# Optimization experiments

Measured on AMD Instinct MI355X. Metric: run time of the kernel, lower is better.

Reference implementation:

```python
import jax, jax.numpy as jnp
import numpy as np

B, N, N_IN, MSG_HID, MSG_OUT, N_HID, N_OUT, K = 32, 128, 16, 64, 64, 64, 16, 4
E = N * (N - 1)  # 16256 directed edges, fully connected w/o self-loops


def setup_inputs() -> dict:
    key = jax.random.key(0)
    ks = jax.random.split(key, 8)
    # one-hot relation matrices (NRI convention)
    rows, cols = np.where(np.ones((N, N)) - np.eye(N))
    eye = np.eye(N, dtype=np.float32)
    rel_rec = jnp.asarray(eye[rows])   # [E, N]
    rel_send = jnp.asarray(eye[cols])  # [E, N]
    s = 0.1  # weight init scale
    return {
        "inputs": jax.random.normal(ks[0], (B, N_IN, N), jnp.float32),
        "rel_rec": rel_rec,
        "rel_send": rel_send,
        "rel_types": jax.nn.softmax(jax.random.normal(ks[1], (B, E, K), jnp.float32), axis=-1),
        "W1": jax.random.normal(ks[2], (K, 2 * N_IN, MSG_HID), jnp.float32) * s,
        "b1": jnp.zeros((K, MSG_HID), jnp.float32),
        "W2": jax.random.normal(ks[3], (K, MSG_HID, MSG_OUT), jnp.float32) * s,
        "b2": jnp.zeros((K, MSG_OUT), jnp.float32),
        "Wo1": jax.random.normal(ks[4], (MSG_OUT + N_IN, N_HID), jnp.float32) * s,
        "bo1": jnp.zeros((N_HID,), jnp.float32),
        "Wo2": jax.random.normal(ks[5], (N_HID, N_HID), jnp.float32) * s,
        "bo2": jnp.zeros((N_HID,), jnp.float32),
        "Wo3": jax.random.normal(ks[6], (N_HID, N_OUT), jnp.float32) * s,
        "bo3": jnp.zeros((N_OUT,), jnp.float32),
    }


def reference(inputs, rel_rec, rel_send, rel_types, W1, b1, W2, b2, Wo1, bo1, Wo2, bo2, Wo3, bo3):
    x = jnp.transpose(inputs, (0, 2, 1))                     # [B, N, n_in]
    senders = jnp.einsum('en,bnf->bef', rel_send, x)          # [B, E, n_in]
    receivers = jnp.einsum('en,bnf->bef', rel_rec, x)         # [B, E, n_in]
    pre_msg = jnp.concatenate([senders, receivers], axis=-1)  # [B, E, 2*n_in]
    all_msgs = jnp.zeros((pre_msg.shape[0], pre_msg.shape[1], W2.shape[-1]), pre_msg.dtype)
    for k in range(W1.shape[0]):  # small fixed loop over edge types
        m = jax.nn.relu(pre_msg @ W1[k] + b1[k])
        m = jax.nn.relu(m @ W2[k] + b2[k])
        all_msgs = all_msgs + m * rel_types[:, :, k:k + 1]
    # edge2node aggregation (no normalization in forward path, matches source)
    agg_msgs = jnp.einsum('bem,en->bnm', all_msgs, rel_rec)   # [B, N, msg_out]
    aug_msgs = jnp.concatenate([x, agg_msgs], axis=-1)        # [B, N, n_in+msg_out]
    h = jax.nn.relu(aug_msgs @ Wo1 + bo1)  # dropout disabled (eval mode)
    h = jax.nn.relu(h @ Wo2 + bo2)
    pred = h @ Wo3 + bo3                                      # [B, N, n_out]
    return jnp.transpose(pred, (0, 2, 1))                     # [B, n_out, N]
```

## Files before the change

kernel.cpp:

```cpp
#include <hip/hip_runtime.h>
#include <stdint.h>

#define B_  32
#define N_  128
#define NIN 16
#define K_  4
#define E_  (N_*(N_-1))

typedef float    f4 __attribute__((ext_vector_type(4)));
typedef _Float16 h8 __attribute__((ext_vector_type(8)));
typedef _Float16 h4 __attribute__((ext_vector_type(4)));

__global__ __launch_bounds__(256) void prep(
    const float* __restrict__ inp, const float* __restrict__ W1,
    const float* __restrict__ b1,  const float* __restrict__ W2,
    const float* __restrict__ Wo1, const float* __restrict__ Wo2,
    const float* __restrict__ Wo3, const float* __restrict__ rt,
    _Float16* __restrict__ Sh, _Float16* __restrict__ Rh,
    _Float16* __restrict__ w2h, _Float16* __restrict__ wn,
    float* __restrict__ rtf)
{
    const int bid = blockIdx.x;
    const int tid = threadIdx.x;
    if (bid < 1024) {
        int gid = bid*256 + tid;
        int c0 = (gid & 15)*4;
        int n  = (gid >> 4) & 127;
        int b  = (gid >> 11) & 31;
        int k  = gid >> 16;
        f4 s = {0.f,0.f,0.f,0.f};
        f4 r = *(const f4*)(b1 + k*64 + c0);
        const float* xp  = inp + (b*NIN)*N_ + n;
        const f4* w1s = (const f4*)(W1 + (k*32)*64 + c0);
        const f4* w1r = (const f4*)(W1 + (k*32 + 16)*64 + c0);
        #pragma unroll
        for (int f = 0; f < 16; ++f) {
            float xv = xp[f*N_];
            s += xv * w1s[f*16];
            r += xv * w1r[f*16];
        }
        int base = ((k*B_ + b)*N_ + n)*64 + c0;
        h4 sh, rh;
        #pragma unroll
        for (int u = 0; u < 4; ++u) { sh[u] = (_Float16)s[u]; rh[u] = (_Float16)r[u]; }
        *(h4*)(Sh + base) = sh;
        *(h4*)(Rh + base) = rh;
    } else if (bid < 1088) {
        int t = (bid - 1024)*256 + tid;
        int i    = t & 7;
        int lane = (t >> 3) & 63;
        int nt   = (t >> 9) & 3;
        int ks   = (t >> 11) & 1;
        int k    = t >> 12;
        int c = ks*32 + (lane >> 4)*8 + i;
        int o = nt*16 + (lane & 15);
        w2h[t] = (_Float16)W2[(k*64 + c)*64 + o];
    } else if (bid < 1132) {
        int t = (bid - 1088)*256 + tid;
        int j    = t & 7;
        int lane = (t >> 3) & 63;
        int f    = t >> 9;
        int col = lane & 15, q = lane >> 4, row = q*8 + j;
        float v;
        if (f < 12) {
            int ks = f >> 2, nt = f & 3, i = ks*32 + row;
            v = (i < 80) ? Wo1[i*64 + nt*16 + col] : 0.f;
        } else if (f < 20) {
            int g = f - 12, ks = g >> 2, nt = g & 3, i = ks*32 + row;
            v = Wo2[i*64 + nt*16 + col];
        } else {
            int ks = f - 20, i = ks*32 + row;
            v = Wo3[i*16 + col];
        }
        wn[t] = (_Float16)v;
    } else {
        int t = (bid - 1132)*256 + tid;
        int jg = t & 31;
        int r  = (t >> 5) & 127;
        int b  = t >> 12;
        const f4* rt4p = (const f4*)(rt + (size_t)(b*E_ + r*127)*4);
        #pragma unroll
        for (int u = 0; u < 4; ++u) {
            int j = jg*4 + u;
            if (j < 127) {
                f4 v = rt4p[j];
                int s = j + (j >= r ? 1 : 0);
                #pragma unroll
                for (int k = 0; k < 4; ++k)
                    rtf[(size_t)((k*B_ + b)*N_ + r)*N_ + s] = v[k];
            } else {
                #pragma unroll
                for (int k = 0; k < 4; ++k)
                    rtf[(size_t)((k*B_ + b)*N_ + r)*N_ + r] = 0.f;
            }
        }
    }
}

__global__ __launch_bounds__(256) void edge_mfma(
    const _Float16* __restrict__ Sh, const _Float16* __restrict__ Rh,
    const _Float16* __restrict__ w2h, const float* __restrict__ rtf,
    const float* __restrict__ b2, float* __restrict__ aggK)
{
    __shared__ _Float16 Rlh[16*64];
    __shared__ float    Rtf[16*128];
    __shared__ float    aggW[2][2][8][64];

    const int tid  = threadIdx.x;
    const int wave = tid >> 6;
    const int lane = tid & 63;
    const int col  = lane & 15;
    const int q    = lane >> 4;
    const int h    = wave & 1;
    const int p    = wave >> 1;
    const int bid  = blockIdx.x;
    const int re   = bid & 7;
    const int b    = (bid >> 3) & 31;
    const int k    = bid >> 8;
    const int kb   = k*B_ + b;
    const int r0   = re*16;

    if (tid < 128)
        *(h8*)(Rlh + tid*8) = *(const h8*)(Rh + ((size_t)kb*N_ + r0)*64 + tid*8);
    {
        const float* src = rtf + ((size_t)kb*N_ + r0)*N_;
        *(f4*)(Rtf + tid*4)        = *(const f4*)(src + tid*4);
        *(f4*)(Rtf + 1024 + tid*4) = *(const f4*)(src + 1024 + tid*4);
    }

    h8 sf[4][2];
    const _Float16* Sg = Sh + ((size_t)kb*N_ + h*64)*64;
    #pragma unroll
    for (int mt = 0; mt < 4; ++mt) {
        sf[mt][0] = *(const h8*)(Sg + (mt*16 + col)*64 + q*8);
        sf[mt][1] = *(const h8*)(Sg + (mt*16 + col)*64 + (4 + q)*8);
    }

    const h8* w2v = (const h8*)w2h;
    h8 w2f[2][4];
    #pragma unroll
    for (int ks = 0; ks < 2; ++ks)
        #pragma unroll
        for (int nt = 0; nt < 4; ++nt)
            w2f[ks][nt] = w2v[((k*2 + ks)*4 + nt)*64 + lane];

    f4 b2i[4];
    #pragma unroll
    for (int nt = 0; nt < 4; ++nt) {
        float v = b2[k*64 + nt*16 + col];
        b2i[nt][0] = v; b2i[nt][1] = v; b2i[nt][2] = v; b2i[nt][3] = v;
    }

    __syncthreads();

    const h8 zero8 = {0,0,0,0,0,0,0,0};
    const f4 zero4 = {0.f,0.f,0.f,0.f};

    #pragma unroll 1
    for (int rg = 0; rg < 8; ++rg) {
        const int rl = p*8 + rg;
        h8 rf0 = *(const h8*)(Rlh + rl*64 + q*8);
        h8 rf1 = *(const h8*)(Rlh + rl*64 + (4 + q)*8);

        f4 vacc[4] = {zero4, zero4, zero4, zero4};
        #pragma unroll
        for (int mt = 0; mt < 4; ++mt) {
            f4 rt4 = *(const f4*)(Rtf + rl*128 + h*64 + mt*16 + q*4);
            h8 a0 = __builtin_elementwise_max(sf[mt][0] + rf0, zero8);
            h8 a1 = __builtin_elementwise_max(sf[mt][1] + rf1, zero8);

            #pragma unroll
            for (int nt = 0; nt < 4; ++nt) {
                f4 acc = __builtin_amdgcn_mfma_f32_16x16x32_f16(a0, w2f[0][nt], b2i[nt], 0, 0, 0);
                acc     = __builtin_amdgcn_mfma_f32_16x16x32_f16(a1, w2f[1][nt], acc,    0, 0, 0);
                f4 m = __builtin_elementwise_max(acc, zero4);
                vacc[nt] += rt4 * m;
            }
        }
        #pragma unroll
        for (int nt = 0; nt < 4; ++nt) {
            float v = vacc[nt][0] + vacc[nt][1] + vacc[nt][2] + vacc[nt][3];
            v += __shfl_xor(v, 16, 64);
            v += __shfl_xor(v, 32, 64);
            if (lane < 16) aggW[p][h][rg][nt*16 + lane] = v;
        }
    }
    __syncthreads();

    {
        int rl = tid >> 4, c4 = tid & 15;
        f4 v = *(const f4*)(&aggW[rl >> 3][0][rl & 7][c4*4])
             + *(const f4*)(&aggW[rl >> 3][1][rl & 7][c4*4]);
        *(f4*)(aggK + ((size_t)kb*N_ + r0 + rl)*64 + c4*4) = v;
    }
}

__global__ __launch_bounds__(256) void node_mfma(
    const float* __restrict__ aggK, const float* __restrict__ inp,
    const _Float16* __restrict__ wn,
    const float* __restrict__ bo1, const float* __restrict__ bo2,
    const float* __restrict__ bo3, float* __restrict__ out)
{
    __shared__ _Float16 augH[64*128];
    __shared__ _Float16 h12[64*64];

    const int tid = threadIdx.x;
    const int b   = blockIdx.x >> 1;
    const int r0  = (blockIdx.x & 1)*64;

    {
        const int nl = tid >> 2, c4 = tid & 3;
        const int r  = r0 + nl;
        float xv[4];
        #pragma unroll
        for (int u = 0; u < 4; ++u)
            xv[u] = inp[(b*NIN + c4*4 + u)*N_ + r];
        f4 av[4];
        #pragma unroll
        for (int w = 0; w < 4; ++w) {
            int c = w*16 + c4*4;
            f4 a = {0.f,0.f,0.f,0.f};
            #pragma unroll
            for (int k = 0; k < 4; ++k)
                a += *(const f4*)(aggK + (((size_t)k*B_ + b)*N_ + r)*64 + c);
            av[w] = a;
        }
        #pragma unroll
        for (int u = 0; u < 4; ++u) {
            int i = c4*4 + u;
            augH[nl*128 + (((i>>3) ^ (nl&15))<<3) + (i&7)] = (_Float16)xv[u];
        }
        #pragma unroll
        for (int w = 0; w < 4; ++w)
            #pragma unroll
            for (int u = 0; u < 4; ++u) {
                int i = 16 + w*16 + c4*4 + u;
                augH[nl*128 + (((i>>3) ^ (nl&15))<<3) + (i&7)] = (_Float16)av[w][u];
            }
        if (c4 < 2)
            #pragma unroll
            for (int u = 0; u < 8; ++u) {
                int i = 80 + c4*8 + u;
                augH[nl*128 + (((i>>3) ^ (nl&15))<<3) + (i&7)] = (_Float16)0.f;
            }
    }
    __syncthreads();

    const int mt  = tid >> 6, lane = tid & 63;
    const int col = lane & 15, q = lane >> 4;
    const h8* wv   = (const h8*)wn;
    const h8* augV = (const h8*)augH;
    const h8* hv   = (const h8*)h12;
    const int nl   = mt*16 + col;

    f4 acc[4];
    #pragma unroll
    for (int nt = 0; nt < 4; ++nt) {
        float v = bo1[nt*16 + col];
        acc[nt][0] = v; acc[nt][1] = v; acc[nt][2] = v; acc[nt][3] = v;
    }
    #pragma unroll
    for (int ks = 0; ks < 3; ++ks) {
        h8 af = augV[nl*16 + ((ks*4 + q) ^ col)];
        #pragma unroll
        for (int nt = 0; nt < 4; ++nt)
            acc[nt] = __builtin_amdgcn_mfma_f32_16x16x32_f16(af, wv[(ks*4 + nt)*64 + lane], acc[nt], 0, 0, 0);
    }
    #pragma unroll
    for (int nt = 0; nt < 4; ++nt)
        #pragma unroll
        for (int i = 0; i < 4; ++i) {
            int n2 = mt*16 + q*4 + i, o = nt*16 + col;
            h12[n2*64 + (((o>>3) ^ (n2&7))<<3) + (o&7)] = (_Float16)fmaxf(acc[nt][i], 0.f);
        }

    f4 acc2[4];
    #pragma unroll
    for (int nt = 0; nt < 4; ++nt) {
        float v = bo2[nt*16 + col];
        acc2[nt][0] = v; acc2[nt][1] = v; acc2[nt][2] = v; acc2[nt][3] = v;
    }
    #pragma unroll
    for (int ks = 0; ks < 2; ++ks) {
        h8 af = hv[nl*8 + ((ks*4 + q) ^ (col & 7))];
        #pragma unroll
        for (int nt = 0; nt < 4; ++nt)
            acc2[nt] = __builtin_amdgcn_mfma_f32_16x16x32_f16(af, wv[(12 + ks*4 + nt)*64 + lane], acc2[nt], 0, 0, 0);
    }
    #pragma unroll
    for (int nt = 0; nt < 4; ++nt)
        #pragma unroll
        for (int i = 0; i < 4; ++i) {
            int n2 = mt*16 + q*4 + i, o = nt*16 + col;
            h12[n2*64 + (((o>>3) ^ (n2&7))<<3) + (o&7)] = (_Float16)fmaxf(acc2[nt][i], 0.f);
        }

    f4 acc3;
    {
        float v = bo3[col];
        acc3[0] = v; acc3[1] = v; acc3[2] = v; acc3[3] = v;
    }
    #pragma unroll
    for (int ks = 0; ks < 2; ++ks) {
        h8 af = hv[nl*8 + ((ks*4 + q) ^ (col & 7))];
        acc3 = __builtin_amdgcn_mfma_f32_16x16x32_f16(af, wv[(20 + ks)*64 + lane], acc3, 0, 0, 0);
    }
    #pragma unroll
    for (int i = 0; i < 4; ++i) {
        int r = r0 + mt*16 + q*4 + i;
        out[(b*NIN + col)*N_ + r] = acc3[i];
    }
}

extern "C" void kernel_launch(void* const* d_in, const int* in_sizes, int n_in,
                              void* d_out, int out_size, void* d_ws, size_t ws_size,
                              hipStream_t stream)
{
    const float* inp = (const float*)d_in[0];
    const float* rt  = (const float*)d_in[3];
    const float* W1  = (const float*)d_in[4];
    const float* b1  = (const float*)d_in[5];
    const float* W2  = (const float*)d_in[6];
    const float* b2  = (const float*)d_in[7];
    const float* Wo1 = (const float*)d_in[8];
    const float* bo1 = (const float*)d_in[9];
    const float* Wo2 = (const float*)d_in[10];
    const float* bo2 = (const float*)d_in[11];
    const float* Wo3 = (const float*)d_in[12];
    const float* bo3 = (const float*)d_in[13];

    _Float16* Sh   = (_Float16*)d_ws;
    _Float16* Rh   = Sh + (1u << 20);
    _Float16* w2h  = Rh + (1u << 20);
    _Float16* wn   = w2h + 16384;
    float*    rtf  = (float*)(wn + 11264);
    float*    aggK = rtf + (1u << 21);

    hipLaunchKernelGGL(prep, dim3(1644), dim3(256), 0, stream,
                       inp, W1, b1, W2, Wo1, Wo2, Wo3, rt, Sh, Rh, w2h, wn, rtf);
    hipLaunchKernelGGL(edge_mfma, dim3(1024), dim3(256), 0, stream,
                       Sh, Rh, w2h, rtf, b2, aggK);
    hipLaunchKernelGGL(node_mfma, dim3(64), dim3(256), 0, stream,
                       aggK, inp, wn, bo1, bo2, bo3, (float*)d_out);
}
```

Measured before the change: 134.6 us.

## Fuse prep stage into edge and node kernels, recompute projections per block

Removes the separate prep kernel and its global-memory intermediates (fp16 sender/receiver projections, repacked weights and the scattered rel_types tensor). Each edge block now stages x, W1 and W2 in shared memory, computes the first-layer projections with MFMA, and scatters rel_types straight into LDS. The node kernel transposes and converts its own weights into LDS. This saves a launch and global round-trips, but every block redundantly recomputes the sender projections and weight conversions, and uses more LDS, which may lower occupancy.

```diff
diff --git a/kernel.cpp b/kernel.cpp
--- a/kernel.cpp
+++ b/kernel.cpp
@@ -9,100 +9,18 @@
 
 typedef float    f4 __attribute__((ext_vector_type(4)));
 typedef _Float16 h8 __attribute__((ext_vector_type(8)));
-typedef _Float16 h4 __attribute__((ext_vector_type(4)));
-
-__global__ __launch_bounds__(256) void prep(
+
+__global__ __launch_bounds__(256) void edge_fused(
     const float* __restrict__ inp, const float* __restrict__ W1,
     const float* __restrict__ b1,  const float* __restrict__ W2,
-    const float* __restrict__ Wo1, const float* __restrict__ Wo2,
-    const float* __restrict__ Wo3, const float* __restrict__ rt,
-    _Float16* __restrict__ Sh, _Float16* __restrict__ Rh,
-    _Float16* __restrict__ w2h, _Float16* __restrict__ wn,
-    float* __restrict__ rtf)
+    const float* __restrict__ b2,  const float* __restrict__ rt,
+    float* __restrict__ aggK)
 {
-    const int bid = blockIdx.x;
-    const int tid = threadIdx.x;
-    if (bid < 1024) {
-        int gid = bid*256 + tid;
-        int c0 = (gid & 15)*4;
-        int n  = (gid >> 4) & 127;
-        int b  = (gid >> 11) & 31;
-        int k  = gid >> 16;
-        f4 s = {0.f,0.f,0.f,0.f};
-        f4 r = *(const f4*)(b1 + k*64 + c0);
-        const float* xp  = inp + (b*NIN)*N_ + n;
-        const f4* w1s = (const f4*)(W1 + (k*32)*64 + c0);
-        const f4* w1r = (const f4*)(W1 + (k*32 + 16)*64 + c0);
-        #pragma unroll
-        for (int f = 0; f < 16; ++f) {
-            float xv = xp[f*N_];
-            s += xv * w1s[f*16];
-            r += xv * w1r[f*16];
-        }
-        int base = ((k*B_ + b)*N_ + n)*64 + c0;
-        h4 sh, rh;
-        #pragma unroll
-        for (int u = 0; u < 4; ++u) { sh[u] = (_Float16)s[u]; rh[u] = (_Float16)r[u]; }
-        *(h4*)(Sh + base) = sh;
-        *(h4*)(Rh + base) = rh;
-    } else if (bid < 1088) {
-        int t = (bid - 1024)*256 + tid;
-        int i    = t & 7;
-        int lane = (t >> 3) & 63;
-        int nt   = (t >> 9) & 3;
-        int ks   = (t >> 11) & 1;
-        int k    = t >> 12;
-        int c = ks*32 + (lane >> 4)*8 + i;
-        int o = nt*16 + (lane & 15);
-        w2h[t] = (_Float16)W2[(k*64 + c)*64 + o];
-    } else if (bid < 1132) {
-        int t = (bid - 1088)*256 + tid;
-        int j    = t & 7;
-        int lane = (t >> 3) & 63;
-        int f    = t >> 9;
-        int col = lane & 15, q = lane >> 4, row = q*8 + j;
-        float v;
-        if (f < 12) {
-            int ks = f >> 2, nt = f & 3, i = ks*32 + row;
-            v = (i < 80) ? Wo1[i*64 + nt*16 + col] : 0.f;
-        } else if (f < 20) {
-            int g = f - 12, ks = g >> 2, nt = g & 3, i = ks*32 + row;
-            v = Wo2[i*64 + nt*16 + col];
-        } else {
-            int ks = f - 20, i = ks*32 + row;
-            v = Wo3[i*16 + col];
-        }
-        wn[t] = (_Float16)v;
-    } else {
-        int t = (bid - 1132)*256 + tid;
-        int jg = t & 31;
-        int r  = (t >> 5) & 127;
-        int b  = t >> 12;
-        const f4* rt4p = (const f4*)(rt + (size_t)(b*E_ + r*127)*4);
-        #pragma unroll
-        for (int u = 0; u < 4; ++u) {
-            int j = jg*4 + u;
-            if (j < 127) {
-                f4 v = rt4p[j];
-                int s = j + (j >= r ? 1 : 0);
-                #pragma unroll
-                for (int k = 0; k < 4; ++k)
-                    rtf[(size_t)((k*B_ + b)*N_ + r)*N_ + s] = v[k];
-            } else {
-                #pragma unroll
-                for (int k = 0; k < 4; ++k)
-                    rtf[(size_t)((k*B_ + b)*N_ + r)*N_ + r] = 0.f;
-            }
-        }
-    }
-}
-
-__global__ __launch_bounds__(256) void edge_mfma(
-    const _Float16* __restrict__ Sh, const _Float16* __restrict__ Rh,
-    const _Float16* __restrict__ w2h, const float* __restrict__ rtf,
-    const float* __restrict__ b2, float* __restrict__ aggK)
-{
-    __shared__ _Float16 Rlh[16*64];
+    __shared__ _Float16 xh[128*16];
+    __shared__ _Float16 w1t[64*32];
+    __shared__ _Float16 w2t[64*64];
+    __shared__ _Float16 Ssw[128*64];
+    __shared__ _Float16 Rl[16*64];
     __shared__ float    Rtf[16*128];
     __shared__ float    aggW[2][2][8][64];
 
@@ -111,8 +29,6 @@
     const int lane = tid & 63;
     const int col  = lane & 15;
     const int q    = lane >> 4;
-    const int h    = wave & 1;
-    const int p    = wave >> 1;
     const int bid  = blockIdx.x;
     const int re   = bid & 7;
     const int b    = (bid >> 3) & 31;
@@ -120,29 +36,45 @@
     const int kb   = k*B_ + b;
     const int r0   = re*16;
 
-    if (tid < 128)
-        *(h8*)(Rlh + tid*8) = *(const h8*)(Rh + ((size_t)kb*N_ + r0)*64 + tid*8);
-    {
-        const float* src = rtf + ((size_t)kb*N_ + r0)*N_;
-        *(f4*)(Rtf + tid*4)        = *(const f4*)(src + tid*4);
-        *(f4*)(Rtf + 1024 + tid*4) = *(const f4*)(src + 1024 + tid*4);
-    }
-
-    h8 sf[4][2];
-    const _Float16* Sg = Sh + ((size_t)kb*N_ + h*64)*64;
-    #pragma unroll
-    for (int mt = 0; mt < 4; ++mt) {
-        sf[mt][0] = *(const h8*)(Sg + (mt*16 + col)*64 + q*8);
-        sf[mt][1] = *(const h8*)(Sg + (mt*16 + col)*64 + (4 + q)*8);
-    }
-
-    const h8* w2v = (const h8*)w2h;
-    h8 w2f[2][4];
-    #pragma unroll
-    for (int ks = 0; ks < 2; ++ks)
-        #pragma unroll
-        for (int nt = 0; nt < 4; ++nt)
-            w2f[ks][nt] = w2v[((k*2 + ks)*4 + nt)*64 + lane];
+    const h8 zero8 = {0,0,0,0,0,0,0,0};
+    const f4 zero4 = {0.f,0.f,0.f,0.f};
+
+    const float* inpB = inp + b*NIN*N_;
+    #pragma unroll
+    for (int rep = 0; rep < 8; ++rep) {
+        int idx = rep*256 + tid;
+        int f = idx >> 7, n = idx & 127;
+        xh[n*16 + f] = (_Float16)inpB[f*N_ + n];
+    }
+    const float* W1k = W1 + k*32*64;
+    #pragma unroll
+    for (int rep = 0; rep < 8; ++rep) {
+        int idx = rep*256 + tid;
+        int kk = idx >> 6, c = idx & 63;
+        w1t[c*32 + kk] = (_Float16)W1k[idx];
+    }
+    const float* W2k = W2 + k*64*64;
+    #pragma unroll
+    for (int rep = 0; rep < 16; ++rep) {
+        int idx = rep*256 + tid;
+        int cc = idx >> 6, o = idx & 63;
+        w2t[o*64 + cc] = (_Float16)W2k[idx];
+    }
+    {
+        int rl = tid >> 4, c16 = tid & 15;
+        int r  = r0 + rl;
+        const float* rowp = rt + ((size_t)(b*E_ + r*127))*4 + k;
+        #pragma unroll
+        for (int u = 0; u < 8; ++u) {
+            int j = c16*8 + u;
+            if (j < 127) {
+                float v = rowp[j*4];
+                int s = j + (j >= r ? 1 : 0);
+                Rtf[rl*128 + s] = v;
+            }
+        }
+        if (c16 == 0) Rtf[rl*128 + r] = 0.f;
+    }
 
     f4 b2i[4];
     #pragma unroll
@@ -150,25 +82,82 @@
         float v = b2[k*64 + nt*16 + col];
         b2i[nt][0] = v; b2i[nt][1] = v; b2i[nt][2] = v; b2i[nt][3] = v;
     }
-
     __syncthreads();
 
-    const h8 zero8 = {0,0,0,0,0,0,0,0};
-    const f4 zero4 = {0.f,0.f,0.f,0.f};
+    {
+        h8 bsf[4], brf[4];
+        #pragma unroll
+        for (int nt = 0; nt < 4; ++nt) {
+            bsf[nt] = zero8; brf[nt] = zero8;
+            if (q < 2) {
+                bsf[nt] = *(const h8*)(w1t + (nt*16 + col)*32 + q*8);
+                brf[nt] = *(const h8*)(w1t + (nt*16 + col)*32 + 16 + q*8);
+            }
+        }
+        f4 b1i[4];
+        #pragma unroll
+        for (int nt = 0; nt < 4; ++nt) {
+            float v = b1[k*64 + nt*16 + col];
+            b1i[nt][0] = v; b1i[nt][1] = v; b1i[nt][2] = v; b1i[nt][3] = v;
+        }
+        #pragma unroll
+        for (int u = 0; u < 2; ++u) {
+            int ms = wave*2 + u;
+            h8 af = zero8;
+            if (q < 2) af = *(const h8*)(xh + (ms*16 + col)*16 + q*8);
+            #pragma unroll
+            for (int nt = 0; nt < 4; ++nt) {
+                f4 acc = __builtin_amdgcn_mfma_f32_16x16x32_f16(af, bsf[nt], zero4, 0, 0, 0);
+                #pragma unroll
+                for (int i = 0; i < 4; ++i) {
+                    int s = ms*16 + q*4 + i, c = nt*16 + col;
+                    Ssw[(s*8 + ((c >> 3) ^ (s & 7)))*8 + (c & 7)] = (_Float16)acc[i];
+                }
+            }
+            if (ms == re) {
+                #pragma unroll
+                for (int nt = 0; nt < 4; ++nt) {
+                    f4 acc = __builtin_amdgcn_mfma_f32_16x16x32_f16(af, brf[nt], b1i[nt], 0, 0, 0);
+                    #pragma unroll
+                    for (int i = 0; i < 4; ++i)
+                        Rl[(q*4 + i)*64 + nt*16 + col] = (_Float16)acc[i];
+                }
+            }
+        }
+    }
+
+    h8 w2f[2][4];
+    #pragma unroll
+    for (int ks = 0; ks < 2; ++ks)
+        #pragma unroll
+        for (int nt = 0; nt < 4; ++nt)
+            w2f[ks][nt] = *(const h8*)(w2t + (nt*16 + col)*64 + ks*32 + q*8);
+
+    __syncthreads();
+
+    const int hh = wave & 1;
+    const int p  = wave >> 1;
+
+    h8 sf[4][2];
+    #pragma unroll
+    for (int mt = 0; mt < 4; ++mt) {
+        int s = hh*64 + mt*16 + col;
+        sf[mt][0] = *(const h8*)(Ssw + (s*8 + (q       ^ (s & 7)))*8);
+        sf[mt][1] = *(const h8*)(Ssw + (s*8 + ((4 + q) ^ (s & 7)))*8);
+    }
 
     #pragma unroll 1
     for (int rg = 0; rg < 8; ++rg) {
         const int rl = p*8 + rg;
-        h8 rf0 = *(const h8*)(Rlh + rl*64 + q*8);
-        h8 rf1 = *(const h8*)(Rlh + rl*64 + (4 + q)*8);
+        h8 rf0 = *(const h8*)(Rl + rl*64 + q*8);
+        h8 rf1 = *(const h8*)(Rl + rl*64 + (4 + q)*8);
 
         f4 vacc[4] = {zero4, zero4, zero4, zero4};
         #pragma unroll
         for (int mt = 0; mt < 4; ++mt) {
-            f4 rt4 = *(const f4*)(Rtf + rl*128 + h*64 + mt*16 + q*4);
+            f4 rt4 = *(const f4*)(Rtf + rl*128 + hh*64 + mt*16 + q*4);
             h8 a0 = __builtin_elementwise_max(sf[mt][0] + rf0, zero8);
             h8 a1 = __builtin_elementwise_max(sf[mt][1] + rf1, zero8);
-
             #pragma unroll
             for (int nt = 0; nt < 4; ++nt) {
                 f4 acc = __builtin_amdgcn_mfma_f32_16x16x32_f16(a0, w2f[0][nt], b2i[nt], 0, 0, 0);
@@ -182,7 +171,7 @@
             float v = vacc[nt][0] + vacc[nt][1] + vacc[nt][2] + vacc[nt][3];
             v += __shfl_xor(v, 16, 64);
             v += __shfl_xor(v, 32, 64);
-            if (lane < 16) aggW[p][h][rg][nt*16 + lane] = v;
+            if (lane < 16) aggW[p][hh][rg][nt*16 + lane] = v;
         }
     }
     __syncthreads();
@@ -197,10 +186,14 @@
 
 __global__ __launch_bounds__(256) void node_mfma(
     const float* __restrict__ aggK, const float* __restrict__ inp,
-    const _Float16* __restrict__ wn,
-    const float* __restrict__ bo1, const float* __restrict__ bo2,
-    const float* __restrict__ bo3, float* __restrict__ out)
+    const float* __restrict__ Wo1, const float* __restrict__ bo1,
+    const float* __restrict__ Wo2, const float* __restrict__ bo2,
+    const float* __restrict__ Wo3, const float* __restrict__ bo3,
+    float* __restrict__ out)
 {
+    __shared__ _Float16 won1t[64*96];
+    __shared__ _Float16 won2t[64*64];
+    __shared__ _Float16 won3t[16*64];
     __shared__ _Float16 augH[64*128];
     __shared__ _Float16 h12[64*64];
 
@@ -208,6 +201,31 @@
     const int b   = blockIdx.x >> 1;
     const int r0  = (blockIdx.x & 1)*64;
 
+    #pragma unroll
+    for (int rep = 0; rep < 20; ++rep) {
+        int idx = rep*256 + tid;
+        int i = idx >> 6, o = idx & 63;
+        won1t[o*96 + i] = (_Float16)Wo1[idx];
+    }
+    #pragma unroll
+    for (int rep = 0; rep < 4; ++rep) {
+        int idx = rep*256 + tid;
+        int o = idx >> 4, i = 80 + (idx & 15);
+        won1t[o*96 + i] = (_Float16)0.f;
+    }
+    #pragma unroll
+    for (int rep = 0; rep < 16; ++rep) {
+        int idx = rep*256 + tid;
+        int i = idx >> 6, o = idx & 63;
+        won2t[o*64 + i] = (_Float16)Wo2[idx];
+    }
+    #pragma unroll
+    for (int rep = 0; rep < 4; ++rep) {
+        int idx = rep*256 + tid;
+        int i = idx >> 4, o = idx & 15;
+        won3t[o*64 + i] = (_Float16)Wo3[idx];
+    }
+
     {
         const int nl = tid >> 2, c4 = tid & 3;
         const int r  = r0 + nl;
@@ -248,7 +266,6 @@
 
     const int mt  = tid >> 6, lane = tid & 63;
     const int col = lane & 15, q = lane >> 4;
-    const h8* wv   = (const h8*)wn;
     const h8* augV = (const h8*)augH;
     const h8* hv   = (const h8*)h12;
     const int nl   = mt*16 + col;
@@ -263,8 +280,10 @@
     for (int ks = 0; ks < 3; ++ks) {
         h8 af = augV[nl*16 + ((ks*4 + q) ^ col)];
         #pragma unroll
-        for (int nt = 0; nt < 4; ++nt)
-            acc[nt] = __builtin_amdgcn_mfma_f32_16x16x32_f16(af, wv[(ks*4 + nt)*64 + lane], acc[nt], 0, 0, 0);
+        for (int nt = 0; nt < 4; ++nt) {
+            h8 wb = *(const h8*)(won1t + (nt*16 + col)*96 + ks*32 + q*8);
+            acc[nt] = __builtin_amdgcn_mfma_f32_16x16x32_f16(af, wb, acc[nt], 0, 0, 0);
+        }
     }
     #pragma unroll
     for (int nt = 0; nt < 4; ++nt)
@@ -284,8 +303,10 @@
     for (int ks = 0; ks < 2; ++ks) {
         h8 af = hv[nl*8 + ((ks*4 + q) ^ (col & 7))];
         #pragma unroll
-        for (int nt = 0; nt < 4; ++nt)
-            acc2[nt] = __builtin_amdgcn_mfma_f32_16x16x32_f16(af, wv[(12 + ks*4 + nt)*64 + lane], acc2[nt], 0, 0, 0);
+        for (int nt = 0; nt < 4; ++nt) {
+            h8 wb = *(const h8*)(won2t + (nt*16 + col)*64 + ks*32 + q*8);
+            acc2[nt] = __builtin_amdgcn_mfma_f32_16x16x32_f16(af, wb, acc2[nt], 0, 0, 0);
+        }
     }
     #pragma unroll
     for (int nt = 0; nt < 4; ++nt)
@@ -303,7 +324,8 @@
     #pragma unroll
     for (int ks = 0; ks < 2; ++ks) {
         h8 af = hv[nl*8 + ((ks*4 + q) ^ (col & 7))];
-        acc3 = __builtin_amdgcn_mfma_f32_16x16x32_f16(af, wv[(20 + ks)*64 + lane], acc3, 0, 0, 0);
+        h8 wb = *(const h8*)(won3t + col*64 + ks*32 + q*8);
+        acc3 = __builtin_amdgcn_mfma_f32_16x16x32_f16(af, wb, acc3, 0, 0, 0);
     }
     #pragma unroll
     for (int i = 0; i < 4; ++i) {
@@ -329,17 +351,10 @@
     const float* Wo3 = (const float*)d_in[12];
     const float* bo3 = (const float*)d_in[13];
 
-    _Float16* Sh   = (_Float16*)d_ws;
-    _Float16* Rh   = Sh + (1u << 20);
-    _Float16* w2h  = Rh + (1u << 20);
-    _Float16* wn   = w2h + 16384;
-    float*    rtf  = (float*)(wn + 11264);
-    float*    aggK = rtf + (1u << 21);
-
-    hipLaunchKernelGGL(prep, dim3(1644), dim3(256), 0, stream,
-                       inp, W1, b1, W2, Wo1, Wo2, Wo3, rt, Sh, Rh, w2h, wn, rtf);
-    hipLaunchKernelGGL(edge_mfma, dim3(1024), dim3(256), 0, stream,
-                       Sh, Rh, w2h, rtf, b2, aggK);
+    float* aggK = (float*)d_ws;
+
+    hipLaunchKernelGGL(edge_fused, dim3(1024), dim3(256), 0, stream,
+                       inp, W1, b1, W2, b2, rt, aggK);
     hipLaunchKernelGGL(node_mfma, dim3(64), dim3(256), 0, stream,
-                       aggK, inp, wn, bo1, bo2, bo3, (float*)d_out);
+                       aggK, inp, Wo1, bo1, Wo2, bo2, Wo3, bo3, (float*)d_out);
 }
```

After: 136.8 us. No clear change (+1.6%).
